# Optimization experiments

Hardware: AMD Instinct MI355X
Metric: run time of the kernel (lower is better)

Reference implementation:

```python
import jax, jax.numpy as jnp
import numpy as np


def setup_inputs() -> dict:
    key = jax.random.key(0)
    ks = jax.random.split(key, 6)
    B, H, W, C = 2, 96, 96, 64
    x = jax.random.normal(ks[0], (B, H, W, C), dtype=jnp.float32)
    # 1x1 conv weights as [C_in, C_out] matrices (kernel size 1)
    W1 = jax.random.normal(ks[1], (C, C // 8), dtype=jnp.float32) * 0.1
    b1 = jnp.zeros((C // 8,), dtype=jnp.float32)
    W2 = jax.random.normal(ks[2], (C, C // 8), dtype=jnp.float32) * 0.1
    b2 = jnp.zeros((C // 8,), dtype=jnp.float32)
    W3 = jax.random.normal(ks[3], (C, C // 2), dtype=jnp.float32) * 0.1
    b3 = jnp.zeros((C // 2,), dtype=jnp.float32)
    W4 = jax.random.normal(ks[4], (C // 2, C), dtype=jnp.float32) * 0.1
    b4 = jnp.zeros((C,), dtype=jnp.float32)
    gamma = jax.random.uniform(ks[5], (1,), dtype=jnp.float32)
    return {"x": x, "W1": W1, "b1": b1, "W2": W2, "b2": b2,
            "W3": W3, "b3": b3, "W4": W4, "b4": b4, "gamma": gamma}


def reference(x, W1, b1, W2, b2, W3, b3, W4, b4, gamma):
    B, H, W_, C = x.shape
    N = H * W_
    # 1x1 convs == per-pixel matmuls
    f = jnp.einsum('bhwc,cd->bhwd', x, W1) + b1   # [B,H,W,C/8] (key)
    g = jnp.einsum('bhwc,cd->bhwd', x, W2) + b2   # [B,H,W,C/8] (query)
    h = jnp.einsum('bhwc,cd->bhwd', x, W3) + b3   # [B,H,W,C/2] (value)
    f = f.reshape(B, N, -1)
    g = g.reshape(B, N, -1)
    h = h.reshape(B, N, -1)
    s = jnp.einsum('bnd,bmd->bnm', g, f)          # [B,N,N] full score matrix
    beta = jax.nn.softmax(s, axis=-1)
    o = jnp.einsum('bnm,bmd->bnd', beta, h)       # [B,N,C/2]
    o = o.reshape(B, H, W_, C // 2)
    o = jnp.einsum('bhwc,cd->bhwd', o, W4) + b4   # [B,H,W,C]
    return gamma[0] * o + x
```

## Files before the change

### kernel.cpp

```cpp
#include <hip/hip_runtime.h>
#include <hip/hip_bf16.h>


#define BATCH 2
#define NTOK 9216
#define CCH 64
#define DV 32
#define KS 8
#define KEYS_PER_BLOCK (NTOK / KS)
#define KEYS_PER_WAVE (KEYS_PER_BLOCK / 4)
#define KT 32
#define NKT (KEYS_PER_WAVE / KT)
#define ROWS (BATCH * NTOK)
#define QTB (ROWS / 64)
#define NKTILE (NTOK / 32)
#define LOG2E 1.44269504088896340736f
#define PB 32
#define XPAD 68
#define ZTOT 152064

typedef __attribute__((ext_vector_type(8))) short bf16x8;
typedef __attribute__((ext_vector_type(4))) float f32x4;

__device__ __forceinline__ short f2bf(float x) {
    __hip_bfloat16 h = __float2bfloat16(x);
    return *(short*)&h;
}
__device__ __forceinline__ float bf2f(short s) {
    unsigned u = ((unsigned)(unsigned short)s) << 16;
    return *(float*)&u;
}

__global__ __launch_bounds__(512) void proj_kernel(
    const float* __restrict__ x,
    const float* __restrict__ W1, const float* __restrict__ b1,
    const float* __restrict__ W2, const float* __restrict__ b2,
    const float* __restrict__ W3, const float* __restrict__ b3,
    short* __restrict__ fx, short* __restrict__ gx, short* __restrict__ hTi,
    float4* __restrict__ zbase)
{
    __shared__ float xS[PB * XPAD];
    __shared__ short fgS[2][PB][32];
    __shared__ short hS[32][PB + 2];

    const int tid = threadIdx.x;
    const int r0  = blockIdx.x * PB;

    {
        int zi = blockIdx.x * 512 + tid;
        if (zi < ZTOT) zbase[zi] = make_float4(0.f, 0.f, 0.f, 0.f);
    }

    {
        const int row = tid >> 4, c4 = tid & 15;
        ((float4*)(xS + row * XPAD))[c4] =
            ((const float4*)(x + (size_t)(r0 + row) * CCH))[c4];
    }
    __syncthreads();

    {
        const int half = tid >> 8;
        const int rr   = (tid & 255) >> 3;
        const int c    = tid & 7;
        const float* xr = xS + rr * XPAD;
        if (half == 0) {
            float acc = b1[c];
            #pragma unroll
            for (int k = 0; k < CCH; ++k) acc += xr[k] * W1[k * 8 + c];
            short hi = f2bf(acc);
            short lo = f2bf(acc - bf2f(hi));
            fgS[0][rr][c] = hi; fgS[0][rr][c + 8] = hi;
            fgS[0][rr][c + 16] = lo; fgS[0][rr][c + 24] = 0;
        } else {
            float acc = b2[c];
            #pragma unroll
            for (int k = 0; k < CCH; ++k) acc += xr[k] * W2[k * 8 + c];
            acc *= LOG2E;
            short hi = f2bf(acc);
            short lo = f2bf(acc - bf2f(hi));
            fgS[1][rr][c] = hi; fgS[1][rr][c + 8] = lo;
            fgS[1][rr][c + 16] = hi; fgS[1][rr][c + 24] = 0;
        }
    }
    {
        const int c = tid & 31;
        const int rbase = tid >> 5;
        #pragma unroll
        for (int s = 0; s < 2; ++s) {
            int rr = rbase + s * 16;
            float acc = b3[c];
            #pragma unroll
            for (int k = 0; k < CCH; ++k) acc += xS[rr * XPAD + k] * W3[k * 32 + c];
            int np = ((rr & 15) >> 2) * 8 + (rr & 3) + ((rr >> 4) & 1) * 4;
            hS[c][np] = f2bf(acc);
        }
    }
    __syncthreads();

    ((int*)(fx + (size_t)r0 * 32))[tid] = ((const int*)fgS[0])[tid];
    ((int*)(gx + (size_t)r0 * 32))[tid] = ((const int*)fgS[1])[tid];
    {
        const int b  = r0 / NTOK;
        const int n0 = r0 - b * NTOK;
        const int kt = n0 >> 5;
        const int c  = tid >> 4;
        const int d  = tid & 15;
        ((int*)(hTi + ((size_t)(b * NKTILE + kt)) * 1024))[c * 16 + d] =
            ((const int*)&hS[c][0])[d];
    }
}

__global__ __launch_bounds__(256, 4) void attn_kernel(
    const short* __restrict__ fx, const short* __restrict__ gx,
    const short* __restrict__ hTi,
    float* __restrict__ l_acc, float* __restrict__ o_acc)
{
    __shared__ float red[64 * 33];

    const int tid  = threadIdx.x;
    const int wave = tid >> 6;
    const int lane = tid & 63;
    const int col  = lane & 15;
    const int quad = lane >> 4;

    const int blk = blockIdx.x;
    const int qt  = blk % QTB;
    const int ks  = blk / QTB;
    const int b   = qt / (QTB / BATCH);
    const int qbase   = (qt % (QTB / BATCH)) * 64;
    const int rowbase = b * NTOK + qbase;

    const bf16x8 agA = *(const bf16x8*)(gx + (size_t)(rowbase + col) * 32 + quad * 8);
    const bf16x8 agB = *(const bf16x8*)(gx + (size_t)(rowbase + 16 + col) * 32 + quad * 8);
    const bf16x8 agC = *(const bf16x8*)(gx + (size_t)(rowbase + 32 + col) * 32 + quad * 8);
    const bf16x8 agD = *(const bf16x8*)(gx + (size_t)(rowbase + 48 + col) * 32 + quad * 8);

    bf16x8 ones;
    #pragma unroll
    for (int j = 0; j < 8; ++j) ones[j] = (short)0x3F80;

    f32x4 oA0 = {0,0,0,0}, oA1 = {0,0,0,0};
    f32x4 oB0 = {0,0,0,0}, oB1 = {0,0,0,0};
    f32x4 oC0 = {0,0,0,0}, oC1 = {0,0,0,0};
    f32x4 oD0 = {0,0,0,0}, oD1 = {0,0,0,0};
    f32x4 lfA = {0,0,0,0}, lfB = {0,0,0,0};
    f32x4 lfC = {0,0,0,0}, lfD = {0,0,0,0};
    const f32x4 zero4 = {0,0,0,0};

    const int kstart = ks * KEYS_PER_BLOCK + wave * KEYS_PER_WAVE;
    const short* fbase = fx + ((size_t)b * NTOK + kstart) * 32;
    const short* hbase = hTi + ((size_t)(b * NKTILE) + (kstart >> 5)) * 1024
                             + col * 32 + quad * 8;

    bf16x8 fa0 = *(const bf16x8*)(fbase + (size_t)col * 32 + quad * 8);
    bf16x8 fa1 = *(const bf16x8*)(fbase + (size_t)(16 + col) * 32 + quad * 8);
    bf16x8 hb0 = *(const bf16x8*)(hbase);
    bf16x8 hb1 = *(const bf16x8*)(hbase + 512);

    union PU { int i[4]; bf16x8 v; };

    #define EXPPACK(T0, T1, P)                                                  \
    {                                                                           \
        float e0 = __builtin_amdgcn_exp2f(T0[0]), e1 = __builtin_amdgcn_exp2f(T0[1]); \
        float e2 = __builtin_amdgcn_exp2f(T0[2]), e3 = __builtin_amdgcn_exp2f(T0[3]); \
        float e4 = __builtin_amdgcn_exp2f(T1[0]), e5 = __builtin_amdgcn_exp2f(T1[1]); \
        float e6 = __builtin_amdgcn_exp2f(T1[2]), e7 = __builtin_amdgcn_exp2f(T1[3]); \
        P.i[0] = (int)__builtin_amdgcn_perm((unsigned)__float_as_int(e1) + 0x8000u, \
                                            (unsigned)__float_as_int(e0) + 0x8000u, 0x07060302u); \
        P.i[1] = (int)__builtin_amdgcn_perm((unsigned)__float_as_int(e3) + 0x8000u, \
                                            (unsigned)__float_as_int(e2) + 0x8000u, 0x07060302u); \
        P.i[2] = (int)__builtin_amdgcn_perm((unsigned)__float_as_int(e5) + 0x8000u, \
                                            (unsigned)__float_as_int(e4) + 0x8000u, 0x07060302u); \
        P.i[3] = (int)__builtin_amdgcn_perm((unsigned)__float_as_int(e7) + 0x8000u, \
                                            (unsigned)__float_as_int(e6) + 0x8000u, 0x07060302u); \
    }

    for (int t = 0; t < NKT; ++t) {
        f32x4 tA0 = __builtin_amdgcn_mfma_f32_16x16x32_bf16(fa0, agA, zero4, 0, 0, 0);
        f32x4 tA1 = __builtin_amdgcn_mfma_f32_16x16x32_bf16(fa1, agA, zero4, 0, 0, 0);
        f32x4 tB0 = __builtin_amdgcn_mfma_f32_16x16x32_bf16(fa0, agB, zero4, 0, 0, 0);
        f32x4 tB1 = __builtin_amdgcn_mfma_f32_16x16x32_bf16(fa1, agB, zero4, 0, 0, 0);
        f32x4 tC0 = __builtin_amdgcn_mfma_f32_16x16x32_bf16(fa0, agC, zero4, 0, 0, 0);
        f32x4 tC1 = __builtin_amdgcn_mfma_f32_16x16x32_bf16(fa1, agC, zero4, 0, 0, 0);
        f32x4 tD0 = __builtin_amdgcn_mfma_f32_16x16x32_bf16(fa0, agD, zero4, 0, 0, 0);
        f32x4 tD1 = __builtin_amdgcn_mfma_f32_16x16x32_bf16(fa1, agD, zero4, 0, 0, 0);

        const int kn = (t + 1 < NKT) ? (t + 1) : 0;
        bf16x8 nf0 = *(const bf16x8*)(fbase + (size_t)(kn * KT + col) * 32 + quad * 8);
        bf16x8 nf1 = *(const bf16x8*)(fbase + (size_t)(kn * KT + 16 + col) * 32 + quad * 8);
        bf16x8 nh0 = *(const bf16x8*)(hbase + kn * 1024);
        bf16x8 nh1 = *(const bf16x8*)(hbase + kn * 1024 + 512);

        PU pA, pB, pC, pD;
        EXPPACK(tA0, tA1, pA)
        EXPPACK(tB0, tB1, pB)
        oA0 = __builtin_amdgcn_mfma_f32_16x16x32_bf16(pA.v, hb0, oA0, 0, 0, 0);
        oA1 = __builtin_amdgcn_mfma_f32_16x16x32_bf16(pA.v, hb1, oA1, 0, 0, 0);
        lfA = __builtin_amdgcn_mfma_f32_16x16x32_bf16(pA.v, ones, lfA, 0, 0, 0);
        oB0 = __builtin_amdgcn_mfma_f32_16x16x32_bf16(pB.v, hb0, oB0, 0, 0, 0);
        oB1 = __builtin_amdgcn_mfma_f32_16x16x32_bf16(pB.v, hb1, oB1, 0, 0, 0);
        lfB = __builtin_amdgcn_mfma_f32_16x16x32_bf16(pB.v, ones, lfB, 0, 0, 0);
        EXPPACK(tC0, tC1, pC)
        EXPPACK(tD0, tD1, pD)
        oC0 = __builtin_amdgcn_mfma_f32_16x16x32_bf16(pC.v, hb0, oC0, 0, 0, 0);
        oC1 = __builtin_amdgcn_mfma_f32_16x16x32_bf16(pC.v, hb1, oC1, 0, 0, 0);
        lfC = __builtin_amdgcn_mfma_f32_16x16x32_bf16(pC.v, ones, lfC, 0, 0, 0);
        oD0 = __builtin_amdgcn_mfma_f32_16x16x32_bf16(pD.v, hb0, oD0, 0, 0, 0);
        oD1 = __builtin_amdgcn_mfma_f32_16x16x32_bf16(pD.v, hb1, oD1, 0, 0, 0);
        lfD = __builtin_amdgcn_mfma_f32_16x16x32_bf16(pD.v, ones, lfD, 0, 0, 0);

        fa0 = nf0; fa1 = nf1; hb0 = nh0; hb1 = nh1;
    }
    #undef EXPPACK

    for (int w = 1; w < 4; ++w) {
        if (wave == w) {
            #pragma unroll
            for (int r = 0; r < 4; ++r) {
                int q = quad * 4 + r;
                red[(q)      * 33 + col]      = oA0[r];
                red[(q)      * 33 + 16 + col] = oA1[r];
                red[(q + 16) * 33 + col]      = oB0[r];
                red[(q + 16) * 33 + 16 + col] = oB1[r];
                red[(q + 32) * 33 + col]      = oC0[r];
                red[(q + 32) * 33 + 16 + col] = oC1[r];
                red[(q + 48) * 33 + col]      = oD0[r];
                red[(q + 48) * 33 + 16 + col] = oD1[r];
            }
            if (col == 0) {
                #pragma unroll
                for (int r = 0; r < 4; ++r) {
                    int q = quad * 4 + r;
                    red[(q)      * 33 + 32] = lfA[r];
                    red[(q + 16) * 33 + 32] = lfB[r];
                    red[(q + 32) * 33 + 32] = lfC[r];
                    red[(q + 48) * 33 + 32] = lfD[r];
                }
            }
        }
        __syncthreads();
        if (wave == 0) {
            #pragma unroll
            for (int r = 0; r < 4; ++r) {
                int q = quad * 4 + r;
                oA0[r] += red[(q)      * 33 + col];
                oA1[r] += red[(q)      * 33 + 16 + col];
                oB0[r] += red[(q + 16) * 33 + col];
                oB1[r] += red[(q + 16) * 33 + 16 + col];
                oC0[r] += red[(q + 32) * 33 + col];
                oC1[r] += red[(q + 32) * 33 + 16 + col];
                oD0[r] += red[(q + 48) * 33 + col];
                oD1[r] += red[(q + 48) * 33 + 16 + col];
                lfA[r] += red[(q)      * 33 + 32];
                lfB[r] += red[(q + 16) * 33 + 32];
                lfC[r] += red[(q + 32) * 33 + 32];
                lfD[r] += red[(q + 48) * 33 + 32];
            }
        }
        __syncthreads();
    }
    if (wave == 0) {
        #pragma unroll
        for (int r = 0; r < 4; ++r) {
            int q = quad * 4 + r;
            atomicAdd(&o_acc[(size_t)(rowbase + q)      * 32 + col],      oA0[r]);
            atomicAdd(&o_acc[(size_t)(rowbase + q)      * 32 + 16 + col], oA1[r]);
            atomicAdd(&o_acc[(size_t)(rowbase + q + 16) * 32 + col],      oB0[r]);
            atomicAdd(&o_acc[(size_t)(rowbase + q + 16) * 32 + 16 + col], oB1[r]);
            atomicAdd(&o_acc[(size_t)(rowbase + q + 32) * 32 + col],      oC0[r]);
            atomicAdd(&o_acc[(size_t)(rowbase + q + 32) * 32 + 16 + col], oC1[r]);
            atomicAdd(&o_acc[(size_t)(rowbase + q + 48) * 32 + col],      oD0[r]);
            atomicAdd(&o_acc[(size_t)(rowbase + q + 48) * 32 + 16 + col], oD1[r]);
        }
        if (col == 0) {
            #pragma unroll
            for (int r = 0; r < 4; ++r) {
                int q = quad * 4 + r;
                atomicAdd(&l_acc[rowbase + q],      lfA[r]);
                atomicAdd(&l_acc[rowbase + q + 16], lfB[r]);
                atomicAdd(&l_acc[rowbase + q + 32], lfC[r]);
                atomicAdd(&l_acc[rowbase + q + 48], lfD[r]);
            }
        }
    }
}

__global__ __launch_bounds__(256) void merge_kernel(
    const float* __restrict__ l_acc, const float* __restrict__ o_acc,
    const float* __restrict__ x,
    const float* __restrict__ W4, const float* __restrict__ b4,
    const float* __restrict__ gamma, float* __restrict__ out)
{
    __shared__ float oS[4][DV];
    int wave = threadIdx.x >> 6;
    int lane = threadIdx.x & 63;
    int row  = blockIdx.x * 4 + wave;

    float invL = 1.f / l_acc[row];
    if (lane < DV) {
        oS[wave][lane] = o_acc[(size_t)row * DV + lane] * invL;
    }
    __syncthreads();

    float dot = b4[lane];
    #pragma unroll
    for (int k = 0; k < DV; ++k) dot += oS[wave][k] * W4[k * 64 + lane];
    float gm  = gamma[0];
    float res = x[(size_t)row * 64 + lane];
    out[(size_t)row * 64 + lane] = gm * dot + res;
}

extern "C" void kernel_launch(void* const* d_in, const int* in_sizes, int n_in,
                              void* d_out, int out_size, void* d_ws, size_t ws_size,
                              hipStream_t stream) {
    const float* x     = (const float*)d_in[0];
    const float* W1    = (const float*)d_in[1];
    const float* b1    = (const float*)d_in[2];
    const float* W2    = (const float*)d_in[3];
    const float* b2    = (const float*)d_in[4];
    const float* W3    = (const float*)d_in[5];
    const float* b3    = (const float*)d_in[6];
    const float* W4    = (const float*)d_in[7];
    const float* b4    = (const float*)d_in[8];
    const float* gamma = (const float*)d_in[9];
    float* out = (float*)d_out;

    short* fx    = (short*)d_ws;
    short* gx    = fx + (size_t)ROWS * 32;
    short* hTi   = gx + (size_t)ROWS * 32;
    float* l_acc = (float*)(hTi + (size_t)ROWS * 32);
    float* o_acc = l_acc + ROWS;

    proj_kernel<<<ROWS / PB, 512, 0, stream>>>(
        x, W1, b1, W2, b2, W3, b3, fx, gx, hTi, (float4*)l_acc);

    attn_kernel<<<QTB * KS, 256, 0, stream>>>(fx, gx, hTi, l_acc, o_acc);

    merge_kernel<<<ROWS / 4, 256, 0, stream>>>(l_acc, o_acc, x, W4, b4, gamma, out);
}
```

Baseline: 127.8 us.

## Halve key splits, vectorize projection LDS reads, truncate exp to bf16

Lowers the key-split factor from 8 to 4, so each block handles twice as many keys. This cuts the partial-result merge work and the number of blocks, at the cost of fewer blocks to fill the GPU. The projection prologue now reads x from shared memory as float4 instead of scalars. The bf16 packing of exp values drops the +0x8000 rounding bias and truncates, which saves four integer adds per pack but adds a small downward bias to the probabilities.

```diff
diff --git a/kernel.cpp b/kernel.cpp
--- a/kernel.cpp
+++ b/kernel.cpp
@@ -6,7 +6,7 @@
 #define NTOK 9216
 #define CCH 64
 #define DV 32
-#define KS 8
+#define KS 4
 #define KEYS_PER_BLOCK (NTOK / KS)
 #define KEYS_PER_WAVE (KEYS_PER_BLOCK / 4)
 #define KT 32
@@ -62,11 +62,15 @@
         const int half = tid >> 8;
         const int rr   = (tid & 255) >> 3;
         const int c    = tid & 7;
-        const float* xr = xS + rr * XPAD;
+        const float4* xr4 = (const float4*)(xS + rr * XPAD);
         if (half == 0) {
             float acc = b1[c];
             #pragma unroll
-            for (int k = 0; k < CCH; ++k) acc += xr[k] * W1[k * 8 + c];
+            for (int k4 = 0; k4 < 16; ++k4) {
+                float4 xv = xr4[k4];
+                acc += xv.x * W1[(4*k4+0) * 8 + c] + xv.y * W1[(4*k4+1) * 8 + c]
+                     + xv.z * W1[(4*k4+2) * 8 + c] + xv.w * W1[(4*k4+3) * 8 + c];
+            }
             short hi = f2bf(acc);
             short lo = f2bf(acc - bf2f(hi));
             fgS[0][rr][c] = hi; fgS[0][rr][c + 8] = hi;
@@ -74,7 +78,11 @@
         } else {
             float acc = b2[c];
             #pragma unroll
-            for (int k = 0; k < CCH; ++k) acc += xr[k] * W2[k * 8 + c];
+            for (int k4 = 0; k4 < 16; ++k4) {
+                float4 xv = xr4[k4];
+                acc += xv.x * W2[(4*k4+0) * 8 + c] + xv.y * W2[(4*k4+1) * 8 + c]
+                     + xv.z * W2[(4*k4+2) * 8 + c] + xv.w * W2[(4*k4+3) * 8 + c];
+            }
             acc *= LOG2E;
             short hi = f2bf(acc);
             short lo = f2bf(acc - bf2f(hi));
@@ -88,9 +96,14 @@
         #pragma unroll
         for (int s = 0; s < 2; ++s) {
             int rr = rbase + s * 16;
+            const float4* xr4 = (const float4*)(xS + rr * XPAD);
             float acc = b3[c];
             #pragma unroll
-            for (int k = 0; k < CCH; ++k) acc += xS[rr * XPAD + k] * W3[k * 32 + c];
+            for (int k4 = 0; k4 < 16; ++k4) {
+                float4 xv = xr4[k4];
+                acc += xv.x * W3[(4*k4+0) * 32 + c] + xv.y * W3[(4*k4+1) * 32 + c]
+                     + xv.z * W3[(4*k4+2) * 32 + c] + xv.w * W3[(4*k4+3) * 32 + c];
+            }
             int np = ((rr & 15) >> 2) * 8 + (rr & 3) + ((rr >> 4) & 1) * 4;
             hS[c][np] = f2bf(acc);
         }
@@ -165,14 +178,14 @@
         float e2 = __builtin_amdgcn_exp2f(T0[2]), e3 = __builtin_amdgcn_exp2f(T0[3]); \
         float e4 = __builtin_amdgcn_exp2f(T1[0]), e5 = __builtin_amdgcn_exp2f(T1[1]); \
         float e6 = __builtin_amdgcn_exp2f(T1[2]), e7 = __builtin_amdgcn_exp2f(T1[3]); \
-        P.i[0] = (int)__builtin_amdgcn_perm((unsigned)__float_as_int(e1) + 0x8000u, \
-                                            (unsigned)__float_as_int(e0) + 0x8000u, 0x07060302u); \
-        P.i[1] = (int)__builtin_amdgcn_perm((unsigned)__float_as_int(e3) + 0x8000u, \
-                                            (unsigned)__float_as_int(e2) + 0x8000u, 0x07060302u); \
-        P.i[2] = (int)__builtin_amdgcn_perm((unsigned)__float_as_int(e5) + 0x8000u, \
-                                            (unsigned)__float_as_int(e4) + 0x8000u, 0x07060302u); \
-        P.i[3] = (int)__builtin_amdgcn_perm((unsigned)__float_as_int(e7) + 0x8000u, \
-                                            (unsigned)__float_as_int(e6) + 0x8000u, 0x07060302u); \
+        P.i[0] = (int)__builtin_amdgcn_perm((unsigned)__float_as_int(e1),       \
+                                            (unsigned)__float_as_int(e0), 0x07060302u); \
+        P.i[1] = (int)__builtin_amdgcn_perm((unsigned)__float_as_int(e3),       \
+                                            (unsigned)__float_as_int(e2), 0x07060302u); \
+        P.i[2] = (int)__builtin_amdgcn_perm((unsigned)__float_as_int(e5),       \
+                                            (unsigned)__float_as_int(e4), 0x07060302u); \
+        P.i[3] = (int)__builtin_amdgcn_perm((unsigned)__float_as_int(e7),       \
+                                            (unsigned)__float_as_int(e6), 0x07060302u); \
     }
 
     for (int t = 0; t < NKT; ++t) {
```

After: 125.7 us. Within noise of the previous version (-1.6%).
